# Kernel optimization log

Measured on AMD Instinct MI355X. Metric: run time of the kernel, lower is better.

Reference implementation:

```python
import jax, jax.numpy as jnp
import numpy as np

K = 3
OFFSET_SCALE = 0.25
GN_GROUPS = 8
GN_EPS = 1e-5


def setup_inputs() -> dict:
    key = jax.random.key(0)
    k1, k2, k3 = jax.random.split(key, 3)
    N, C, H, W = 4, 128, 96, 96
    Cout = 128
    x = jax.random.normal(k1, (N, C, H, W), dtype=jnp.float32)
    # offset head: small random weights so offsets are modest (tanh tames anyway)
    w_head = jax.random.normal(k2, (3, C, 3, 3), dtype=jnp.float32) * 0.05
    b_head = jnp.zeros((3,), dtype=jnp.float32)
    # kaiming-ish scale for the deform conv weight: sqrt(2 / fan_out)
    w_dcn = jax.random.normal(k3, (Cout, C, 3, 3), dtype=jnp.float32) * np.sqrt(2.0 / (Cout * 9))
    gn_gamma = jnp.ones((Cout,), dtype=jnp.float32)
    gn_beta = jnp.zeros((Cout,), dtype=jnp.float32)
    return {"x": x, "w_head": w_head, "b_head": b_head, "w_dcn": w_dcn,
            "gn_gamma": gn_gamma, "gn_beta": gn_beta}


def _conv3x3(x, w, b):
    y = jax.lax.conv_general_dilated(
        x, w, window_strides=(1, 1), padding=((1, 1), (1, 1)),
        dimension_numbers=("NCHW", "OIHW", "NCHW"))
    return y + b[None, :, None, None]


def _deform_sample(xn, py, px):
    # xn: (C,H,W); py/px: (9,H,W) absolute sampling coords (y=row, x=col)
    C, H, W = xn.shape
    y0 = jnp.floor(py).astype(jnp.int32)
    x0 = jnp.floor(px).astype(jnp.int32)
    fy = py - y0
    fx = px - x0
    xf = xn.reshape(C, H * W)

    def corner(yi, xi, wgt):
        valid = (yi >= 0) & (yi < H) & (xi >= 0) & (xi < W)
        idx = jnp.clip(yi, 0, H - 1) * W + jnp.clip(xi, 0, W - 1)  # (9,H,W)
        v = xf[:, idx.reshape(-1)].reshape(C, *idx.shape)  # (C,9,H,W)
        return v * (wgt * valid)[None]

    return (corner(y0, x0, (1 - fy) * (1 - fx))
            + corner(y0, x0 + 1, (1 - fy) * fx)
            + corner(y0 + 1, x0, fy * (1 - fx))
            + corner(y0 + 1, x0 + 1, fy * fx))


def reference(x, w_head, b_head, w_dcn, gn_gamma, gn_beta):
    N, C, H, W = x.shape
    Cout = w_dcn.shape[0]
    stride, pad, dil = 1, 1, 1

    head = _conv3x3(x, w_head, b_head)                 # (N,3,H,W)
    dx, dy, m = head[:, :1], head[:, 1:2], head[:, 2:3]
    mask = jax.nn.sigmoid(m)                           # (N,1,H,W) broadcast over 9 taps
    dx = OFFSET_SCALE * jnp.tanh(dx)
    dy = OFFSET_SCALE * jnp.tanh(dy)

    # serpentine 18-channel offsets, mmcv layout: (oy, ox) pairs per kernel tap
    z = jnp.zeros_like(dx)
    offs = jnp.concatenate(
        [z, z, z, dy, z, -dy, dx, z, z, z, -dx, z, dx, dy, dx, -dy, -dx, dy], axis=1)
    offs = offs.reshape(N, 9, 2, H, W)
    oy, ox = offs[:, :, 0], offs[:, :, 1]              # (N,9,H,W)

    ky = jnp.arange(9) // 3
    kx = jnp.arange(9) % 3
    base_y = (jnp.arange(H) * stride - pad)[None, :, None] + (ky * dil)[:, None, None]
    base_x = (jnp.arange(W) * stride - pad)[None, None, :] + (kx * dil)[:, None, None]
    py = base_y[None] + oy                             # (N,9,H,W)
    px = base_x[None] + ox

    sampled = jax.vmap(_deform_sample)(x, py, px)      # (N,C,9,H,W)
    sampled = sampled * mask[:, None]                  # modulated

    y = jnp.einsum('nckhw,ock->nohw', sampled, w_dcn.reshape(Cout, C, 9))

    # GroupNorm(8, Cout) + ReLU
    G = min(GN_GROUPS, Cout)
    yg = y.reshape(N, G, Cout // G, H, W)
    mu = yg.mean(axis=(2, 3, 4), keepdims=True)
    var = yg.var(axis=(2, 3, 4), keepdims=True)
    yn = ((yg - mu) * jax.lax.rsqrt(var + GN_EPS)).reshape(N, Cout, H, W)
    yn = yn * gn_gamma[None, :, None, None] + gn_beta[None, :, None, None]
    return jax.nn.relu(yn)
```

## Files before the change

kernel.cpp:

```cpp
#include <hip/hip_runtime.h>
#include <hip/hip_bf16.h>
#include <math.h>

#define NB   4
#define CIN  128
#define HH   96
#define WW   96
#define HWN  (HH*WW)
#define NHW  (NB*HWN)
#define COUT 128
#define KW   9
#define KDIM (CIN*KW)
#define GSZ  16
#define PXB  32
#define NBLK (NHW/PXB)

typedef __attribute__((ext_vector_type(8))) short bf16x8;
typedef __attribute__((ext_vector_type(4))) float f32x4;

#define OFF_WAH   0
#define OFF_DX    147456
#define OFF_DY    184320
#define OFF_MASK  221184
#define OFF_GN    258048
#define OFF_MAP   258240
#define OFF_PAIR  258496

__device__ __forceinline__ ushort f2bf(float f) {
    union { float f; uint u; } v; v.f = f;
    uint r = v.u + 0x7fffu + ((v.u >> 16) & 1u);
    return (ushort)(r >> 16);
}
__device__ __forceinline__ float bf2f(ushort h) {
    union { uint u; float f; } v; v.u = ((uint)h) << 16;
    return v.f;
}

__device__ __forceinline__ void barrier_keep_vm() {
    asm volatile("s_waitcnt lgkmcnt(0)\n\ts_barrier" ::: "memory");
}

__global__ __launch_bounds__(256) void pre_kernel(const float* __restrict__ x,
                                                  const float* __restrict__ w_head,
                                                  const float* __restrict__ b_head,
                                                  const float* __restrict__ wd,
                                                  ushort* __restrict__ wah,
                                                  float* __restrict__ dxv,
                                                  float* __restrict__ dyv,
                                                  float* __restrict__ maskv,
                                                  float* __restrict__ gn_part,
                                                  int* __restrict__ map,
                                                  int* __restrict__ pairB) {
    __shared__ float wl[3456];
    __shared__ float sp[4][64][3];
    const int b = blockIdx.x, t = threadIdx.x;

    if (b >= 576) {
        const int bb = b - 576;
        int i = bb * 256 + t;
        {
            int e  = i & 7;
            int l  = (i >> 3) & 63;
            int ot = (i >> 9) & 7;
            int q  = (i >> 12) & 3;
            int k  = i >> 14;
            int o  = ot * 16 + (l & 15);
            int c  = q * 32 + (l >> 4) * 8 + e;
            wah[i] = f2bf(wd[o * KDIM + c * KW + k]);
        }
        if (bb == 0 && t < 128) gn_part[t] = 0.f;
        if (bb == 0 && t < 64) {
            int l = t;
            bf16x8 A1 = {}, B1 = {}, A2 = {}, B2 = {};
            if ((l >> 4) == 0) {
                A1[0] = (short)f2bf((float)((l & 15) + 1));
                B1[0] = (short)f2bf(1.0f);
                A2[0] = (short)f2bf(1.0f);
                B2[0] = (short)f2bf((float)((l & 15) + 1));
            }
            f32x4 d1 = {0.f,0.f,0.f,0.f}, d2 = {0.f,0.f,0.f,0.f};
            d1 = __builtin_amdgcn_mfma_f32_16x16x32_bf16(A1, B1, d1, 0, 0, 0);
            d2 = __builtin_amdgcn_mfma_f32_16x16x32_bf16(A2, B2, d2, 0, 0, 0);
#pragma unroll
            for (int r = 0; r < 4; ++r) {
                int m = (int)(d1[r] + 0.5f) - 1;
                int n = (int)(d2[r] + 0.5f) - 1;
                map[l * 4 + r] = (m << 4) | n;
            }
        }
        if (bb == 1 && t < 64) {
            int l = t;
            union { bf16x8 v; short a[8]; } B;
#pragma unroll
            for (int e = 0; e < 8; ++e) {
                float val = (float)(1u << (((l >> 4) * 8 + e) & 31));
                B.a[e] = (short)f2bf(val);
            }
#pragma unroll
            for (int s = 0; s < 32; ++s) {
                union { bf16x8 v; short a[8]; } A;
#pragma unroll
                for (int e = 0; e < 8; ++e) A.a[e] = 0;
                if ((l >> 4) == (s >> 3)) A.a[s & 7] = (short)f2bf(1.0f);
                f32x4 d = {0.f, 0.f, 0.f, 0.f};
                d = __builtin_amdgcn_mfma_f32_16x16x32_bf16(A.v, B.v, d, 0, 0, 0);
                float v0 = d[0];
                if (l == 0 && v0 > 0.f) {
                    int ex; frexpf(v0, &ex);
                    int j = ex - 1;
                    if (j >= 0 && j < 32) pairB[j] = s;
                }
            }
        }
        return;
    }

    for (int i = t; i < 3456; i += 256) {
        int j = i / KDIM, r = i - j * KDIM;
        wl[r * 3 + j] = w_head[i];
    }
    __syncthreads();

    int lane = t & 63, cg = t >> 6;
    int p = b * 64 + lane;
    int n = p / HWN, hw = p % HWN;
    int h = hw / WW, w = hw % WW;

    int   offs[9];
    float msk[9];
#pragma unroll
    for (int ky = 0; ky < 3; ky++)
#pragma unroll
        for (int kx = 0; kx < 3; kx++) {
            int yy = h - 1 + ky, xx = w - 1 + kx;
            bool ok = (yy >= 0) && (yy < HH) && (xx >= 0) && (xx < WW);
            int yc = min(max(yy, 0), HH - 1), xc = min(max(xx, 0), WW - 1);
            offs[ky * 3 + kx] = yc * WW + xc;
            msk[ky * 3 + kx] = ok ? 1.f : 0.f;
        }

    float a0 = 0.f, a1 = 0.f, a2 = 0.f;
    const float* xn = x + (size_t)n * CIN * HWN;
    for (int c = cg * 32; c < cg * 32 + 32; c++) {
        const float* xc = xn + c * HWN;
        const float* wc = &wl[c * 27];
#pragma unroll
        for (int kk = 0; kk < 9; kk++) {
            float v = xc[offs[kk]] * msk[kk];
            a0 = fmaf(v, wc[kk * 3 + 0], a0);
            a1 = fmaf(v, wc[kk * 3 + 1], a1);
            a2 = fmaf(v, wc[kk * 3 + 2], a2);
        }
    }
    sp[cg][lane][0] = a0; sp[cg][lane][1] = a1; sp[cg][lane][2] = a2;
    __syncthreads();
    if (t < 64) {
        float b0 = sp[0][t][0] + sp[1][t][0] + sp[2][t][0] + sp[3][t][0] + b_head[0];
        float b1 = sp[0][t][1] + sp[1][t][1] + sp[2][t][1] + sp[3][t][1] + b_head[1];
        float b2 = sp[0][t][2] + sp[1][t][2] + sp[2][t][2] + sp[3][t][2] + b_head[2];
        int pp = b * 64 + t;
        dxv[pp]   = 0.25f * tanhf(b0);
        dyv[pp]   = 0.25f * tanhf(b1);
        maskv[pp] = 1.f / (1.f + expf(-b2));
    }
}

__global__ __launch_bounds__(256) void dcn_kernel(const float* __restrict__ x,
                                                  const ushort* __restrict__ wah,
                                                  const float* __restrict__ dxv,
                                                  const float* __restrict__ dyv,
                                                  const float* __restrict__ maskv,
                                                  const int* __restrict__ map,
                                                  const int* __restrict__ pairB,
                                                  float* __restrict__ out,
                                                  float* __restrict__ gn_part) {
    __shared__ __attribute__((aligned(16))) ushort sBh[2][4 * PXB * 8];
    __shared__ float sMask[PXB];
    __shared__ float gred[16];

    const int t = threadIdx.x;
    const int lane = t & 63;
    const int wv = t >> 6;
    const int lg = lane >> 4;
    const int ml = lane & 15;
    const int pix = t & 31;
    const int sg  = t >> 5;

    int b = blockIdx.x;
    int nb = (b & 7) * (NBLK / 8) + (b >> 3);
    const int p0  = nb * PXB;
    const int n   = p0 / HWN;
    const int hw0 = p0 % HWN;
    const float* xn = x + (size_t)n * CIN * HWN;

    if (t < PXB) sMask[t] = maskv[p0 + t];
    if (t < 16) gred[t] = 0.f;

    const float dxl = dxv[p0 + pix];
    const float dyl = dyv[p0 + pix];
    const int hme = (hw0 + pix) / WW;
    const int wme = (hw0 + pix) % WW;

    int chn[4];
#pragma unroll
    for (int e = 0; e < 4; ++e) chn[e] = pairB[sg * 4 + e] & 31;

    f32x4 acc[2][2];
#pragma unroll
    for (int i = 0; i < 2; i++)
#pragma unroll
        for (int j = 0; j < 2; j++) acc[i][j] = (f32x4){0.f, 0.f, 0.f, 0.f};

    const int oyc[9] = {0, 0, 0, 1, 0, -1, 1, 1, -1};
    const int oxc[9] = {0, 1, -1, 0, 0, 0, 1, -1, 1};
    const int ncl[9] = {1, 2, 2, 2, 1, 2, 4, 4, 4};

    int aa[4]; float wq[4];
    float raw[4][4];
    bf16x8 An0, An1;

    {
        float py = (float)(hme - 1), px = (float)(wme - 1);
        float fy0 = floorf(py), fx0 = floorf(px);
        int y0 = (int)fy0, x0 = (int)fx0;
        float fy = py - fy0, fx = px - fx0;
#pragma unroll
        for (int j = 0; j < 4; ++j) {
            int yy = y0 + (j >> 1), xx = x0 + (j & 1);
            float wb = ((j >> 1) ? fy : 1.f - fy) * ((j & 1) ? fx : 1.f - fx);
            bool ok = (yy >= 0) && (yy < HH) && (xx >= 0) && (xx < WW);
            aa[j] = min(max(yy, 0), HH - 1) * WW + min(max(xx, 0), WW - 1);
            wq[j] = ok ? wb : 0.f;
        }
#pragma unroll
        for (int e = 0; e < 4; ++e) raw[e][0] = xn[(size_t)chn[e] * HWN + aa[0]];
        const size_t abase = (size_t)(wv * 2) * 512 + lane * 8;
        An0 = *(const bf16x8*)(wah + abase);
        An1 = *(const bf16x8*)(wah + abase + 512);
    }

#pragma unroll
    for (int j = 0; j < 36; ++j) {
        const int k = j >> 2;
        const int NC = ncl[k];
        bf16x8 Ah0 = An0, Ah1 = An1;
        union { short4 v; ushort u[4]; } hv;
#pragma unroll
        for (int e = 0; e < 4; ++e) {
            float s = raw[e][0] * wq[0];
            if (NC >= 2) s += raw[e][1] * wq[1];
            if (NC == 4) s += raw[e][2] * wq[2] + raw[e][3] * wq[3];
            hv.u[e] = f2bf(s);
        }
        const int wbase = ((sg >> 1) * PXB + pix) * 8 + (sg & 1) * 4;
        *(short4*)&sBh[j & 1][wbase] = hv.v;
        if (j < 35) {
            const int jn = j + 1, kn = jn >> 2, qn = jn & 3;
            if (qn == 0) {
                const int ky = kn / 3, kx = kn - ky * 3;
                float py = (float)(hme - 1 + ky) + (float)oyc[kn] * dxl;
                float px = (float)(wme - 1 + kx) + (float)oxc[kn] * dyl;
                float fy0 = floorf(py), fx0 = floorf(px);
                int y0 = (int)fy0, x0 = (int)fx0;
                float fy = py - fy0, fx = px - fx0;
#pragma unroll
                for (int jj = 0; jj < 4; ++jj) {
                    int yy = y0 + (jj >> 1), xx = x0 + (jj & 1);
                    float wb = ((jj >> 1) ? fy : 1.f - fy) * ((jj & 1) ? fx : 1.f - fx);
                    bool ok = (yy >= 0) && (yy < HH) && (xx >= 0) && (xx < WW);
                    aa[jj] = min(max(yy, 0), HH - 1) * WW + min(max(xx, 0), WW - 1);
                    wq[jj] = ok ? wb : 0.f;
                }
                if (ncl[kn] == 2 && oxc[kn] == 0) { aa[1] = aa[2]; wq[1] = wq[2]; }
            }
            const int NCn = ncl[kn];
            const int ccn = qn * 32;
#pragma unroll
            for (int e = 0; e < 4; ++e) {
                const float* xc = xn + (size_t)(ccn + chn[e]) * HWN;
                raw[e][0] = xc[aa[0]];
                if (NCn >= 2) raw[e][1] = xc[aa[1]];
                if (NCn == 4) { raw[e][2] = xc[aa[2]]; raw[e][3] = xc[aa[3]]; }
            }
            const size_t abase = (size_t)((kn * 4 + qn) * 8 + wv * 2) * 512 + lane * 8;
            An0 = *(const bf16x8*)(wah + abase);
            An1 = *(const bf16x8*)(wah + abase + 512);
        }
        barrier_keep_vm();
#pragma unroll
        for (int pt = 0; pt < 2; ++pt) {
            const int rbase = (lg * PXB + pt * 16 + ml) * 8;
            bf16x8 Bh = *(const bf16x8*)&sBh[j & 1][rbase];
            acc[0][pt] = __builtin_amdgcn_mfma_f32_16x16x32_bf16(Ah0, Bh, acc[0][pt], 0, 0, 0);
            acc[1][pt] = __builtin_amdgcn_mfma_f32_16x16x32_bf16(Ah1, Bh, acc[1][pt], 0, 0, 0);
        }
    }

    int4 mn4 = *(const int4*)&map[lane * 4];
    int mn[4] = {mn4.x, mn4.y, mn4.z, mn4.w};
    float s1g[2] = {0.f, 0.f}, s2g[2] = {0.f, 0.f};
#pragma unroll
    for (int ot = 0; ot < 2; ++ot) {
        int otile = wv * 32 + ot * 16;
#pragma unroll
        for (int pt = 0; pt < 2; ++pt) {
#pragma unroll
            for (int r = 0; r < 4; ++r) {
                int m = mn[r] >> 4, nn2 = mn[r] & 15;
                int p = pt * 16 + nn2;
                float v = acc[ot][pt][r] * sMask[p];
                s1g[ot] += v;
                s2g[ot] += v * v;
                out[((size_t)n * COUT + otile + m) * HWN + hw0 + p] = v;
            }
        }
    }
#pragma unroll
    for (int ot = 0; ot < 2; ++ot) {
        int g = wv * 2 + ot;
        atomicAdd(&gred[g * 2 + 0], s1g[ot]);
        atomicAdd(&gred[g * 2 + 1], s2g[ot]);
    }
    __syncthreads();
    if (t < 8) {
        atomicAdd(&gn_part[n * 8 + t],      gred[t * 2 + 0]);
        atomicAdd(&gn_part[64 + n * 8 + t], gred[t * 2 + 1]);
    }
}

__global__ __launch_bounds__(256) void gn_apply(float* __restrict__ out,
                                                const float* __restrict__ gn_part,
                                                const float* __restrict__ gamma,
                                                const float* __restrict__ beta) {
    int i4 = blockIdx.x * 256 + threadIdx.x;
    size_t e = (size_t)i4 * 4;
    int og = (int)(e / HWN);
    int n = og >> 7, o = og & 127;
    int s = n * 8 + (o >> 4);
    const float cnt = (float)GSZ * (float)HWN;
    float s1 = gn_part[s], s2 = gn_part[64 + s];
    float mu = s1 / cnt;
    float var = s2 / cnt - mu * mu;
    float inv = rsqrtf(var + 1e-5f);
    float ga = gamma[o] * inv;
    float be = beta[o] - mu * ga;
    float4 v = *(float4*)(out + e);
    v.x = fmaxf(fmaf(v.x, ga, be), 0.f);
    v.y = fmaxf(fmaf(v.y, ga, be), 0.f);
    v.z = fmaxf(fmaf(v.z, ga, be), 0.f);
    v.w = fmaxf(fmaf(v.w, ga, be), 0.f);
    *(float4*)(out + e) = v;
}

extern "C" void kernel_launch(void* const* d_in, const int* in_sizes, int n_in,
                              void* d_out, int out_size, void* d_ws, size_t ws_size,
                              hipStream_t stream) {
    const float* x       = (const float*)d_in[0];
    const float* w_head  = (const float*)d_in[1];
    const float* b_head  = (const float*)d_in[2];
    const float* w_dcn   = (const float*)d_in[3];
    const float* gamma   = (const float*)d_in[4];
    const float* beta    = (const float*)d_in[5];
    float* out = (float*)d_out;
    float* ws  = (float*)d_ws;

    ushort* wah    = (ushort*)(ws + OFF_WAH);
    float* dxv     = ws + OFF_DX;
    float* dyv     = ws + OFF_DY;
    float* maskv   = ws + OFF_MASK;
    float* gn_part = ws + OFF_GN;
    int*   map     = (int*)(ws + OFF_MAP);
    int*   pairB   = (int*)(ws + OFF_PAIR);

    pre_kernel<<<1152, 256, 0, stream>>>(x, w_head, b_head, w_dcn, wah,
                                         dxv, dyv, maskv, gn_part, map, pairB);
    dcn_kernel<<<NBLK, 256, 0, stream>>>(x, wah, dxv, dyv, maskv, map, pairB, out, gn_part);
    gn_apply<<<(NB * COUT * HWN) / 4 / 256, 256, 0, stream>>>(out, gn_part, gamma, beta);
}
```

Before: 182.0 us.

## Restructure offset-head conv to register-tile 4 pixels per thread with float4 loads

The 3x3 offset-head convolution now has each thread compute 4 adjacent pixels over 4 channels. It loads a 3x6 input window with float4 loads and reuses it across the 9 taps in registers, instead of doing 9 scalar gathers per pixel. Head weights are repacked with a stride of 28 so they can be read from shared memory as float4, and partial sums are reduced across 32 channel groups in shared memory. Each block now covers 32 pixels, so the grid grows to 1152 head blocks. The cost is more registers and a two-stage shared-memory reduction.

```diff
diff --git a/kernel.cpp b/kernel.cpp
--- a/kernel.cpp
+++ b/kernel.cpp
@@ -26,6 +26,8 @@
 #define OFF_MAP   258240
 #define OFF_PAIR  258496
 
+#define HEADB 1152
+
 __device__ __forceinline__ ushort f2bf(float f) {
     union { float f; uint u; } v; v.f = f;
     uint r = v.u + 0x7fffu + ((v.u >> 16) & 1u);
@@ -51,12 +53,12 @@
                                                   float* __restrict__ gn_part,
                                                   int* __restrict__ map,
                                                   int* __restrict__ pairB) {
-    __shared__ float wl[3456];
-    __shared__ float sp[4][64][3];
+    __shared__ float wl[CIN * 28];
+    __shared__ float sp[32][8][13];
     const int b = blockIdx.x, t = threadIdx.x;
 
-    if (b >= 576) {
-        const int bb = b - 576;
+    if (b >= HEADB) {
+        const int bb = b - HEADB;
         int i = bb * 256 + t;
         {
             int e  = i & 7;
@@ -117,48 +119,90 @@
 
     for (int i = t; i < 3456; i += 256) {
         int j = i / KDIM, r = i - j * KDIM;
-        wl[r * 3 + j] = w_head[i];
+        int c = r / 9, kk = r - c * 9;
+        wl[c * 28 + kk * 3 + j] = w_head[i];
     }
     __syncthreads();
 
-    int lane = t & 63, cg = t >> 6;
-    int p = b * 64 + lane;
-    int n = p / HWN, hw = p % HWN;
-    int h = hw / WW, w = hw % WW;
-
-    int   offs[9];
-    float msk[9];
-#pragma unroll
-    for (int ky = 0; ky < 3; ky++)
-#pragma unroll
-        for (int kx = 0; kx < 3; kx++) {
-            int yy = h - 1 + ky, xx = w - 1 + kx;
-            bool ok = (yy >= 0) && (yy < HH) && (xx >= 0) && (xx < WW);
-            int yc = min(max(yy, 0), HH - 1), xc = min(max(xx, 0), WW - 1);
-            offs[ky * 3 + kx] = yc * WW + xc;
-            msk[ky * 3 + kx] = ok ? 1.f : 0.f;
-        }
-
-    float a0 = 0.f, a1 = 0.f, a2 = 0.f;
+    const int sl = t & 7;
+    const int cg = t >> 3;
+    const int p0 = b * 32 + sl * 4;
+    const int n  = p0 / HWN;
+    const int hw = p0 - n * HWN;
+    const int h  = hw / WW;
+    const int w0 = hw - h * WW;
     const float* xn = x + (size_t)n * CIN * HWN;
-    for (int c = cg * 32; c < cg * 32 + 32; c++) {
-        const float* xc = xn + c * HWN;
-        const float* wc = &wl[c * 27];
-#pragma unroll
-        for (int kk = 0; kk < 9; kk++) {
-            float v = xc[offs[kk]] * msk[kk];
-            a0 = fmaf(v, wc[kk * 3 + 0], a0);
-            a1 = fmaf(v, wc[kk * 3 + 1], a1);
-            a2 = fmaf(v, wc[kk * 3 + 2], a2);
-        }
-    }
-    sp[cg][lane][0] = a0; sp[cg][lane][1] = a1; sp[cg][lane][2] = a2;
+    const bool lok = (w0 > 0);
+    const bool rok = (w0 < WW - 4);
+
+    float acc[12];
+#pragma unroll
+    for (int i = 0; i < 12; ++i) acc[i] = 0.f;
+
+#pragma unroll
+    for (int cc = 0; cc < 4; ++cc) {
+        const int c = cg * 4 + cc;
+        const float* xc = xn + (size_t)c * HWN;
+        float v[3][6];
+#pragma unroll
+        for (int r = 0; r < 3; ++r) {
+            int y = h - 1 + r;
+            if (y >= 0 && y < HH) {
+                const float* xr = xc + y * WW + w0;
+                float4 m4 = *(const float4*)xr;
+                v[r][1] = m4.x; v[r][2] = m4.y; v[r][3] = m4.z; v[r][4] = m4.w;
+                v[r][0] = lok ? xr[-1] : 0.f;
+                v[r][5] = rok ? xr[4]  : 0.f;
+            } else {
+#pragma unroll
+                for (int i = 0; i < 6; ++i) v[r][i] = 0.f;
+            }
+        }
+        float wr[28];
+        const float* wc = &wl[c * 28];
+#pragma unroll
+        for (int i2 = 0; i2 < 7; ++i2) {
+            float4 q4 = *(const float4*)(wc + i2 * 4);
+            wr[i2 * 4 + 0] = q4.x; wr[i2 * 4 + 1] = q4.y;
+            wr[i2 * 4 + 2] = q4.z; wr[i2 * 4 + 3] = q4.w;
+        }
+#pragma unroll
+        for (int ky = 0; ky < 3; ++ky)
+#pragma unroll
+            for (int kx = 0; kx < 3; ++kx) {
+                const int kk = ky * 3 + kx;
+                const float wj0 = wr[kk * 3 + 0];
+                const float wj1 = wr[kk * 3 + 1];
+                const float wj2 = wr[kk * 3 + 2];
+#pragma unroll
+                for (int q = 0; q < 4; ++q) {
+                    float val = v[ky][q + kx];
+                    acc[q * 3 + 0] = fmaf(val, wj0, acc[q * 3 + 0]);
+                    acc[q * 3 + 1] = fmaf(val, wj1, acc[q * 3 + 1]);
+                    acc[q * 3 + 2] = fmaf(val, wj2, acc[q * 3 + 2]);
+                }
+            }
+    }
+#pragma unroll
+    for (int i = 0; i < 12; ++i) sp[cg][sl][i] = acc[i];
     __syncthreads();
-    if (t < 64) {
-        float b0 = sp[0][t][0] + sp[1][t][0] + sp[2][t][0] + sp[3][t][0] + b_head[0];
-        float b1 = sp[0][t][1] + sp[1][t][1] + sp[2][t][1] + sp[3][t][1] + b_head[1];
-        float b2 = sp[0][t][2] + sp[1][t][2] + sp[2][t][2] + sp[3][t][2] + b_head[2];
-        int pp = b * 64 + t;
+    if (cg < 8) {
+#pragma unroll
+        for (int k = 8; k < 32; k += 8)
+#pragma unroll
+            for (int i = 0; i < 12; ++i) sp[cg][sl][i] += sp[cg + k][sl][i];
+    }
+    __syncthreads();
+    if (t < 32) {
+        const int s2 = t >> 2, q = t & 3;
+        float b0 = b_head[0], b1 = b_head[1], b2 = b_head[2];
+#pragma unroll
+        for (int cgi = 0; cgi < 8; ++cgi) {
+            b0 += sp[cgi][s2][q * 3 + 0];
+            b1 += sp[cgi][s2][q * 3 + 1];
+            b2 += sp[cgi][s2][q * 3 + 2];
+        }
+        int pp = b * 32 + t;
         dxv[pp]   = 0.25f * tanhf(b0);
         dyv[pp]   = 0.25f * tanhf(b1);
         maskv[pp] = 1.f / (1.f + expf(-b2));
@@ -372,8 +416,8 @@
     int*   map     = (int*)(ws + OFF_MAP);
     int*   pairB   = (int*)(ws + OFF_PAIR);
 
-    pre_kernel<<<1152, 256, 0, stream>>>(x, w_head, b_head, w_dcn, wah,
-                                         dxv, dyv, maskv, gn_part, map, pairB);
+    pre_kernel<<<HEADB + 576, 256, 0, stream>>>(x, w_head, b_head, w_dcn, wah,
+                                                dxv, dyv, maskv, gn_part, map, pairB);
     dcn_kernel<<<NBLK, 256, 0, stream>>>(x, wah, dxv, dyv, maskv, map, pairB, out, gn_part);
     gn_apply<<<(NB * COUT * HWN) / 4 / 256, 256, 0, stream>>>(out, gn_part, gamma, beta);
 }
```

New measurement: 196.1 us. 7.7% more time.
